# Performance work log

Measured on AMD Instinct MI355X. Metric: run time of the kernel, lower is better.

Reference implementation:

```python
import jax, jax.numpy as jnp
import numpy as np

E = 1024        # embedding_dim
DIN = 2048      # d_inner = E * expand_factor(2)
N = 16          # state_dim
DTR = 64        # dt_rank = ceil(E/16)
K_CONV = 4      # conv_dim


def tt_dense(g1, g2):
    # TT with ranks [1,16,1]: W[(m1,m2),(n1,n2)] = sum_r g1[m1,n1,r] g2[r,m2,n2]
    m1, n1, r = g1.shape
    _, m2, n2 = g2.shape
    return jnp.einsum('air,rbj->abij', g1, g2).reshape(m1 * m2, n1 * n2)


def setup_inputs() -> dict:
    key = jax.random.key(0)
    ks = jax.random.split(key, 12)
    s = 0.05  # init scale for TT cores
    return {
        'x': jax.random.normal(ks[0], (2, 1024, E), dtype=jnp.float32),
        # in_proj: 1024=[32,32] -> 4096=[64,64]
        'in_g1': jax.random.normal(ks[1], (32, 64, 16)) * s,
        'in_g2': jax.random.normal(ks[2], (16, 32, 64)) * s,
        # x_proj: 2048=[32,64] -> 96=[8,12]
        'x_g1': jax.random.normal(ks[3], (32, 8, 16)) * s,
        'x_g2': jax.random.normal(ks[4], (16, 64, 12)) * s,
        # dt_proj: 64=[8,8] -> 2048=[32,64]
        'dt_g1': jax.random.normal(ks[5], (8, 32, 16)) * s,
        'dt_g2': jax.random.normal(ks[6], (16, 8, 64)) * s,
        # out_proj: 2048=[32,64] -> 1024=[32,32]
        'out_g1': jax.random.normal(ks[7], (32, 32, 16)) * s,
        'out_g2': jax.random.normal(ks[8], (16, 64, 32)) * s,
        'conv_filter': jax.random.normal(ks[9], (K_CONV, 1, DIN)) * 0.1,
        'conv_bias': jnp.zeros((DIN,), jnp.float32),
        'A_log': jax.random.uniform(ks[10], (DIN, N), dtype=jnp.float32),
        'D': jnp.zeros((DIN,), jnp.float32),
    }


def _forward(x, in_g1, in_g2, x_g1, x_g2, dt_g1, dt_g2, out_g1, out_g2,
             conv_filter, conv_bias, A_log, D):
    B, L, _ = x.shape
    # in_proj (TT) -> split into conv path and gate
    xz = (x.reshape(-1, E) @ tt_dense(in_g1, in_g2)).reshape(B, L, 2 * DIN)
    x_conv, z = xz[..., :DIN], xz[..., DIN:]
    # depthwise conv1d, SAME padding, + bias, SiLU, gate by z
    conv = jax.lax.conv_general_dilated(
        x_conv, conv_filter, window_strides=(1,), padding='SAME',
        dimension_numbers=('NWC', 'WIO', 'NWC'), feature_group_count=DIN)
    y = jax.nn.silu(conv + conv_bias) * z            # [B, L, DIN]
    # x_proj (TT) -> dt_unscaled, B, C
    dtBC = (y.reshape(-1, DIN) @ tt_dense(x_g1, x_g2)).reshape(B, L, DTR + 2 * N)
    dt_un = dtBC[..., :DTR]
    Bm = dtBC[..., DTR:DTR + N]                      # [B, L, N]
    Cm = dtBC[..., DTR + N:]                         # [B, L, N]
    # dt_proj (TT) + softplus
    dt = jax.nn.softplus(dt_un.reshape(-1, DTR) @ tt_dense(dt_g1, dt_g2)).reshape(B, L, DIN)
    # selective scan
    A = -jnp.exp(A_log)                              # [DIN, N]

    def step(h, inp):
        dt_t, u_t, B_t, C_t = inp                    # [B,DIN],[B,DIN],[B,N],[B,N]
        dA = jnp.exp(dt_t[:, :, None] * A)           # [B, DIN, N]
        h = dA * h + dt_t[:, :, None] * B_t[:, None, :] * u_t[:, :, None]
        y_t = jnp.einsum('bdn,bn->bd', h, C_t) + D * u_t
        return h, (y_t, h)

    h0 = jnp.zeros((B, DIN, N), x.dtype)
    _, (ys, hs) = jax.lax.scan(
        step, h0,
        (dt.swapaxes(0, 1), y.swapaxes(0, 1), Bm.swapaxes(0, 1), Cm.swapaxes(0, 1)))
    ssm_out = ys.swapaxes(0, 1) + jnp.mean(hs) * 1e-8  # [B, L, DIN]
    out = (ssm_out.reshape(-1, DIN) @ tt_dense(out_g1, out_g2)).reshape(B, L, E)
    return out


def reference(x, in_g1, in_g2, x_g1, x_g2, dt_g1, dt_g2, out_g1, out_g2,
              conv_filter, conv_bias, A_log, D):
    return _forward(x, in_g1, in_g2, x_g1, x_g2, dt_g1, dt_g2, out_g1, out_g2,
                    conv_filter, conv_bias, A_log, D)
```

## Files before the change

kernel.cpp:

```cpp
#include <hip/hip_runtime.h>
#include <hip/hip_bf16.h>
#include <cstdint>
#include <cstddef>

#define EE    1024
#define DIN   2048
#define NST   16
#define DTR   64
#define BB_   2
#define LL    1024
#define BL    (BB_*LL)
#define NCHUNK 32
#define CLEN   32
#define RTT   16

typedef unsigned short u16;
typedef unsigned int   u32;

static constexpr size_t OFF_WINT  = 0;
static constexpr size_t OFF_WOUTT = 2097152;
static constexpr size_t OFF_WXT   = 3145728;
static constexpr size_t OFF_WDTT  = 3276800;
static constexpr size_t OFF_A2T   = 3342336;
static constexpr size_t OFF_XB    = 3375104;
static constexpr size_t OFF_XZB   = 4423680;
static constexpr size_t OFF_YB    = 8617984;
static constexpr size_t OFF_PART  = 10715136;
static constexpr size_t OFF_DTBC  = 14909440;
static constexpr size_t OFF_DTUNB = 15106048;
static constexpr size_t OFF_DTB   = 15171584;
static constexpr size_t OFF_YSB   = 17268736;
static constexpr size_t OFF_HC    = 19365888;
static constexpr size_t OFF_SDT   = 21463040;

__device__ __forceinline__ u16 f2bf(float f) {
    u32 u = __float_as_uint(f);
    u += 0x7fffu + ((u >> 16) & 1u);
    return (u16)(u >> 16);
}
__device__ __forceinline__ float bf2f(u16 v) {
    return __uint_as_float((u32)v << 16);
}

__device__ __forceinline__ void async_copy16(const void* g, void* l) {
    __builtin_amdgcn_global_load_lds((const __attribute__((address_space(1))) u32*)g,
                                     (__attribute__((address_space(3))) u32*)l,
                                     16, 0, 0);
}

__device__ __forceinline__ float softplusf(float v) {
    return fmaxf(v, 0.f) + log1pf(__expf(-fabsf(v)));
}

__device__ void tt_part(const float* __restrict__ g1, const float* __restrict__ g2,
                        u16* __restrict__ Wt, int m1, int n1, int m2, int n2,
                        int c, int crows, float* g1col, float* g2col)
{
    const int rowsW = m1 * m2;
    if (c >= crows) {
        for (int k = threadIdx.x; k < rowsW; k += 256)
            Wt[(size_t)c * rowsW + k] = 0;
        return;
    }
    const int i = c / n2;
    const int j = c - i * n2;

    for (int e = threadIdx.x; e < m1 * RTT; e += 256) {
        const int a = e >> 4, rr = e & 15;
        g1col[e] = g1[(size_t)(a * n1 + i) * RTT + rr];
    }
    for (int e = threadIdx.x; e < RTT * m2; e += 256) {
        const int rr = e / m2, bb = e - rr * m2;
        g2col[e] = g2[(size_t)(rr * m2 + bb) * n2 + j];
    }
    __syncthreads();

    for (int k = threadIdx.x; k < rowsW; k += 256) {
        const int a  = k / m2;
        const int bb = k - a * m2;
        const float* gp = g1col + a * RTT;
        float s = 0.f;
        #pragma unroll
        for (int rr = 0; rr < RTT; ++rr)
            s = fmaf(gp[rr], g2col[rr * m2 + bb], s);
        Wt[(size_t)c * rowsW + k] = f2bf(s);
    }
}

__global__ __launch_bounds__(256) void mega_prep(
    const float* __restrict__ in_g1, const float* __restrict__ in_g2, u16* __restrict__ W_inT,
    const float* __restrict__ out_g1, const float* __restrict__ out_g2, u16* __restrict__ W_outT,
    const float* __restrict__ x_g1, const float* __restrict__ x_g2, u16* __restrict__ W_xT,
    const float* __restrict__ dt_g1, const float* __restrict__ dt_g2, u16* __restrict__ W_dtT,
    const float* __restrict__ x, u16* __restrict__ xb,
    const float* __restrict__ A_log, float* __restrict__ A2t)
{
    __shared__ float g1col[32 * RTT];
    __shared__ float g2col[RTT * 64];
    const int blk = blockIdx.x;
    if (blk < 4096) {
        tt_part(in_g1, in_g2, W_inT, 32, 64, 32, 64, blk, 4096, g1col, g2col);
    } else if (blk < 5120) {
        tt_part(out_g1, out_g2, W_outT, 32, 32, 64, 32, blk - 4096, 1024, g1col, g2col);
    } else if (blk < 5248) {
        tt_part(x_g1, x_g2, W_xT, 32, 8, 64, 12, blk - 5120, 96, g1col, g2col);
    } else if (blk < 7296) {
        tt_part(dt_g1, dt_g2, W_dtT, 8, 32, 8, 64, blk - 5248, 2048, g1col, g2col);
    } else if (blk < 9344) {
        const int i = (blk - 7296) * 256 + threadIdx.x;
        float4 v = ((const float4*)x)[i];
        ushort4 o;
        o.x = f2bf(v.x); o.y = f2bf(v.y); o.z = f2bf(v.z); o.w = f2bf(v.w);
        ((ushort4*)xb)[i] = o;
    } else {
        const int idx = (blk - 9344) * 256 + threadIdx.x;
        const int d = idx >> 4, n = idx & 15;
        A2t[n * DIN + d] = -expf(A_log[idx]);
    }
}

typedef __attribute__((ext_vector_type(8))) short bf16x8;
typedef __attribute__((ext_vector_type(4))) float floatx4;

template<int BN, int BK, int OUT>
__global__ __launch_bounds__(256) void gemm_bf16(
    const u16* __restrict__ A, const u16* __restrict__ Bt, void* __restrict__ Cout,
    int K, int ldc, int kchunk, size_t czstride)
{
    constexpr int BM   = 128;
    constexpr int NT   = BN / 32;
    constexpr int SLOT = BK / 8;
    constexpr int CR   = 64 / SLOT;
    constexpr int NACH = BM / CR / 4;
    constexpr int NBCH = BN / CR / 4;
    constexpr int KG   = BK / 32;
    __shared__ u16 As[BM * BK];
    __shared__ u16 Bs[BN * BK];

    const int tid  = threadIdx.x;
    const int w    = tid >> 6;
    const int lane = tid & 63;
    const int wm   = w & 1, wn = w >> 1;
    const int row0 = blockIdx.y * BM;
    const int col0 = blockIdx.x * BN;
    const int kbeg = blockIdx.z * kchunk;

    const int srow = lane / SLOT;
    const int kqp  = lane % SLOT;
    const u16* ga[NACH]; u16* la[NACH];
    #pragma unroll
    for (int i = 0; i < NACH; ++i) {
        const int c  = w * NACH + i;
        const int r  = c * CR + srow;
        const int kq = kqp ^ ((r >> 1) & (SLOT - 1));
        ga[i] = A + (size_t)(row0 + r) * K + kbeg + kq * 8;
        la[i] = &As[c * CR * BK];
    }
    const u16* gb[NBCH]; u16* lb[NBCH];
    #pragma unroll
    for (int i = 0; i < NBCH; ++i) {
        const int c  = w * NBCH + i;
        const int r  = c * CR + srow;
        const int kq = kqp ^ ((r >> 1) & (SLOT - 1));
        gb[i] = Bt + (size_t)(col0 + r) * K + kbeg + kq * 8;
        lb[i] = &Bs[c * CR * BK];
    }

    const int q = lane >> 4, l15 = lane & 15;
    int a_off[4][KG], b_off[NT][KG];
    #pragma unroll
    for (int mt = 0; mt < 4; ++mt) {
        const int r = wm * 64 + mt * 16 + l15;
        const int m = (r >> 1) & (SLOT - 1);
        #pragma unroll
        for (int kk = 0; kk < KG; ++kk)
            a_off[mt][kk] = r * BK + ((kk * 4 + q) ^ m) * 8;
    }
    #pragma unroll
    for (int nt = 0; nt < NT; ++nt) {
        const int r = wn * (BN / 2) + nt * 16 + l15;
        const int m = (r >> 1) & (SLOT - 1);
        #pragma unroll
        for (int kk = 0; kk < KG; ++kk)
            b_off[nt][kk] = r * BK + ((kk * 4 + q) ^ m) * 8;
    }

    floatx4 acc[4][NT];
    #pragma unroll
    for (int mt = 0; mt < 4; ++mt)
        #pragma unroll
        for (int nt = 0; nt < NT; ++nt)
            acc[mt][nt] = (floatx4){0.f, 0.f, 0.f, 0.f};

    for (int k0 = 0; k0 < kchunk; k0 += BK) {
        #pragma unroll
        for (int i = 0; i < NACH; ++i) { async_copy16(ga[i], la[i]); ga[i] += BK; }
        #pragma unroll
        for (int i = 0; i < NBCH; ++i) { async_copy16(gb[i], lb[i]); gb[i] += BK; }
        __syncthreads();

        bf16x8 af[4][KG], bfv[NT][KG];
        #pragma unroll
        for (int mt = 0; mt < 4; ++mt)
            #pragma unroll
            for (int kk = 0; kk < KG; ++kk)
                af[mt][kk] = *(const bf16x8*)&As[a_off[mt][kk]];
        #pragma unroll
        for (int nt = 0; nt < NT; ++nt)
            #pragma unroll
            for (int kk = 0; kk < KG; ++kk)
                bfv[nt][kk] = *(const bf16x8*)&Bs[b_off[nt][kk]];

        #pragma unroll
        for (int kk = 0; kk < KG; ++kk)
            #pragma unroll
            for (int mt = 0; mt < 4; ++mt)
                #pragma unroll
                for (int nt = 0; nt < NT; ++nt)
                    acc[mt][nt] = __builtin_amdgcn_mfma_f32_16x16x32_bf16(
                        af[mt][kk], bfv[nt][kk], acc[mt][nt], 0, 0, 0);

        __syncthreads();
    }

    #pragma unroll
    for (int mt = 0; mt < 4; ++mt) {
        const int row = row0 + wm * 64 + mt * 16 + q * 4;
        #pragma unroll
        for (int nt = 0; nt < NT; ++nt) {
            const int col = col0 + wn * (BN / 2) + nt * 16 + l15;
            #pragma unroll
            for (int r = 0; r < 4; ++r) {
                const float v = acc[mt][nt][r];
                if constexpr (OUT == 0) {
                    ((float*)Cout)[(size_t)blockIdx.z * czstride + (size_t)(row + r) * ldc + col] = v;
                } else if constexpr (OUT == 1) {
                    ((u16*)Cout)[(size_t)(row + r) * ldc + col] = f2bf(v);
                } else {
                    ((u16*)Cout)[(size_t)(row + r) * ldc + col] = f2bf(softplusf(v));
                }
            }
        }
    }
}

__global__ __launch_bounds__(512, 2) void gemm_bf16_dp(
    const u16* __restrict__ A, const u16* __restrict__ Bt, u16* __restrict__ Cout,
    int K, int ldc)
{
    constexpr int BM   = 128;
    constexpr int BN   = 256;
    constexpr int BK   = 64;
    constexpr int SLOT = BK / 8;
    constexpr int CR   = 64 / SLOT;
    constexpr int NACH = BM / CR / 8;
    constexpr int NBCH = BN / CR / 8;
    constexpr int AST  = BM * BK;
    constexpr int BST  = BN * BK;

    __shared__ u16 As[3 * AST];
    __shared__ u16 Bs[3 * BST];

    const int tid  = threadIdx.x;
    const int w    = tid >> 6;
    const int lane = tid & 63;
    const int wm   = w & 1;
    const int wn   = w >> 1;
    const int row0 = blockIdx.y * BM;
    const int col0 = blockIdx.x * BN;

    const int srow = lane / SLOT;
    const int kqp  = lane % SLOT;
    const u16* ga[NACH]; int laA[NACH];
    #pragma unroll
    for (int i = 0; i < NACH; ++i) {
        const int c  = w * NACH + i;
        const int r  = c * CR + srow;
        const int kq = kqp ^ ((r >> 1) & (SLOT - 1));
        ga[i]  = A + (size_t)(row0 + r) * K + kq * 8;
        laA[i] = c * CR * BK;
    }
    const u16* gb[NBCH]; int laB[NBCH];
    #pragma unroll
    for (int i = 0; i < NBCH; ++i) {
        const int c  = w * NBCH + i;
        const int r  = c * CR + srow;
        const int kq = kqp ^ ((r >> 1) & (SLOT - 1));
        gb[i]  = Bt + (size_t)(col0 + r) * K + kq * 8;
        laB[i] = c * CR * BK;
    }

    const int q = lane >> 4, l15 = lane & 15;
    int a_off[4][2], b_off[4][2];
    #pragma unroll
    for (int mt = 0; mt < 4; ++mt) {
        const int r = wm * 64 + mt * 16 + l15;
        const int m = (r >> 1) & (SLOT - 1);
        #pragma unroll
        for (int kk = 0; kk < 2; ++kk)
            a_off[mt][kk] = r * BK + ((kk * 4 + q) ^ m) * 8;
    }
    #pragma unroll
    for (int nt = 0; nt < 4; ++nt) {
        const int r = wn * 64 + nt * 16 + l15;
        const int m = (r >> 1) & (SLOT - 1);
        #pragma unroll
        for (int kk = 0; kk < 2; ++kk)
            b_off[nt][kk] = r * BK + ((kk * 4 + q) ^ m) * 8;
    }

    floatx4 acc[4][4];
    #pragma unroll
    for (int mt = 0; mt < 4; ++mt)
        #pragma unroll
        for (int nt = 0; nt < 4; ++nt)
            acc[mt][nt] = (floatx4){0.f, 0.f, 0.f, 0.f};

    const int NTILES = K / BK;

    #pragma unroll
    for (int i = 0; i < NACH; ++i) { async_copy16(ga[i], &As[0 * AST + laA[i]]); ga[i] += BK; }
    #pragma unroll
    for (int i = 0; i < NBCH; ++i) { async_copy16(gb[i], &Bs[0 * BST + laB[i]]); gb[i] += BK; }
    #pragma unroll
    for (int i = 0; i < NACH; ++i) { async_copy16(ga[i], &As[1 * AST + laA[i]]); ga[i] += BK; }
    #pragma unroll
    for (int i = 0; i < NBCH; ++i) { async_copy16(gb[i], &Bs[1 * BST + laB[i]]); gb[i] += BK; }
    __builtin_amdgcn_sched_barrier(0);
    asm volatile("s_waitcnt vmcnt(6)" ::: "memory");
    __builtin_amdgcn_s_barrier();
    __builtin_amdgcn_sched_barrier(0);

    int cur = 0, nxt = 2;
    for (int t = 0; t < NTILES; ++t) {
        const bool pf = (t + 2 < NTILES);
        const u16* Ac = &As[cur * AST];
        const u16* Bc = &Bs[cur * BST];
        u16* An = &As[nxt * AST];
        u16* Bn = &Bs[nxt * BST];

        bf16x8 af[4], bfv[4];

        #pragma unroll
        for (int mt = 0; mt < 4; ++mt) af[mt]  = *(const bf16x8*)&Ac[a_off[mt][0]];
        #pragma unroll
        for (int nt = 0; nt < 4; ++nt) bfv[nt] = *(const bf16x8*)&Bc[b_off[nt][0]];
        if (pf) {
            async_copy16(ga[0], &An[laA[0]]);
            async_copy16(ga[1], &An[laA[1]]);
            async_copy16(gb[0], &Bn[laB[0]]);
        }
        __builtin_amdgcn_sched_barrier(0);
        __builtin_amdgcn_s_barrier();
        asm volatile("s_waitcnt lgkmcnt(0)" ::: "memory");
        __builtin_amdgcn_sched_barrier(0);
        __builtin_amdgcn_s_setprio(1);
        #pragma unroll
        for (int mt = 0; mt < 4; ++mt)
            #pragma unroll
            for (int nt = 0; nt < 4; ++nt)
                acc[mt][nt] = __builtin_amdgcn_mfma_f32_16x16x32_bf16(
                    af[mt], bfv[nt], acc[mt][nt], 0, 0, 0);
        __builtin_amdgcn_s_setprio(0);
        __builtin_amdgcn_sched_barrier(0);
        __builtin_amdgcn_s_barrier();
        __builtin_amdgcn_sched_barrier(0);

        #pragma unroll
        for (int mt = 0; mt < 4; ++mt) af[mt]  = *(const bf16x8*)&Ac[a_off[mt][1]];
        #pragma unroll
        for (int nt = 0; nt < 4; ++nt) bfv[nt] = *(const bf16x8*)&Bc[b_off[nt][1]];
        if (pf) {
            async_copy16(gb[1], &Bn[laB[1]]);
            async_copy16(gb[2], &Bn[laB[2]]);
            async_copy16(gb[3], &Bn[laB[3]]);
            #pragma unroll
            for (int i = 0; i < NACH; ++i) ga[i] += BK;
            #pragma unroll
            for (int i = 0; i < NBCH; ++i) gb[i] += BK;
        }
        __builtin_amdgcn_sched_barrier(0);
        __builtin_amdgcn_s_barrier();
        asm volatile("s_waitcnt lgkmcnt(0)" ::: "memory");
        __builtin_amdgcn_sched_barrier(0);
        __builtin_amdgcn_s_setprio(1);
        #pragma unroll
        for (int mt = 0; mt < 4; ++mt)
            #pragma unroll
            for (int nt = 0; nt < 4; ++nt)
                acc[mt][nt] = __builtin_amdgcn_mfma_f32_16x16x32_bf16(
                    af[mt], bfv[nt], acc[mt][nt], 0, 0, 0);
        __builtin_amdgcn_s_setprio(0);
        __builtin_amdgcn_sched_barrier(0);
        if (pf) asm volatile("s_waitcnt vmcnt(6)" ::: "memory");
        else    asm volatile("s_waitcnt vmcnt(0)" ::: "memory");
        __builtin_amdgcn_s_barrier();
        __builtin_amdgcn_sched_barrier(0);

        cur = (cur == 2) ? 0 : cur + 1;
        nxt = (nxt == 2) ? 0 : nxt + 1;
    }

    #pragma unroll
    for (int mt = 0; mt < 4; ++mt) {
        const int row = row0 + wm * 64 + mt * 16 + q * 4;
        #pragma unroll
        for (int nt = 0; nt < 4; ++nt) {
            const int col = col0 + wn * 64 + nt * 16 + l15;
            #pragma unroll
            for (int r = 0; r < 4; ++r)
                Cout[(size_t)(row + r) * ldc + col] = f2bf(acc[mt][nt][r]);
        }
    }
}

__global__ __launch_bounds__(256) void reduce_dtbc(
    const float* __restrict__ part, float* __restrict__ dtBC, u16* __restrict__ dtun_b)
{
    int idx = blockIdx.x * 256 + threadIdx.x;
    if (idx >= BL * 96) return;
    const int row = idx / 96;
    const int col = idx - row * 96;
    float s = 0.f;
    #pragma unroll
    for (int z = 0; z < 16; ++z)
        s += part[(size_t)z * BL * 128 + (size_t)row * 128 + col];
    dtBC[idx] = s;
    if (col < 64) dtun_b[(size_t)row * 64 + col] = f2bf(s);
}

__global__ __launch_bounds__(256) void reduce_out(
    const float* __restrict__ part, float* __restrict__ out)
{
    const int idx = blockIdx.x * 256 + threadIdx.x;
    const float4 a = ((const float4*)part)[idx];
    const float4 b = ((const float4*)part)[idx + BL * EE / 4];
    float4 o;
    o.x = a.x + b.x; o.y = a.y + b.y; o.z = a.z + b.z; o.w = a.w + b.w;
    ((float4*)out)[idx] = o;
}

typedef __attribute__((ext_vector_type(8))) unsigned short ushortx8;

__global__ __launch_bounds__(256) void conv_gate(
    const u16* __restrict__ xzb, const float* __restrict__ filt,
    const float* __restrict__ bias, u16* __restrict__ yb)
{
    int idx = blockIdx.x * blockDim.x + threadIdx.x;
    if (idx >= BL * DIN / 8) return;
    const int d  = (idx % (DIN / 8)) * 8;
    const int bt = idx / (DIN / 8);
    const int b  = bt >> 10;
    const int t  = bt & 1023;

    float acc[8];
    #pragma unroll
    for (int j = 0; j < 8; ++j) acc[j] = bias[d + j];
    #pragma unroll
    for (int k = 0; k < 4; ++k) {
        const int tt = t + k - 1;
        if ((unsigned)tt < (unsigned)LL) {
            const ushortx8 xc = *(const ushortx8*)(xzb + (size_t)(b * LL + tt) * (2 * DIN) + d);
            #pragma unroll
            for (int j = 0; j < 8; ++j)
                acc[j] = fmaf(bf2f(xc[j]), filt[(size_t)k * DIN + d + j], acc[j]);
        }
    }
    const ushortx8 z = *(const ushortx8*)(xzb + (size_t)bt * (2 * DIN) + DIN + d);
    ushortx8 o;
    #pragma unroll
    for (int j = 0; j < 8; ++j)
        o[j] = f2bf(acc[j] / (1.f + __expf(-acc[j])) * bf2f(z[j]));
    *(ushortx8*)(yb + (size_t)bt * DIN + d) = o;
}

__global__ __launch_bounds__(256) void scan_phase_a(
    const u16* __restrict__ dt, const u16* __restrict__ u,
    const float* __restrict__ dtBC, const float* __restrict__ A2t,
    float* __restrict__ hend, float* __restrict__ sdtbuf)
{
    const int d = blockIdx.x * 256 + threadIdx.x;
    const int c = blockIdx.y;
    const int b = blockIdx.z;

    __shared__ float Bs[CLEN][NST];
    for (int e = threadIdx.x; e < CLEN * NST; e += 256) {
        const int tl = e >> 4, n = e & 15;
        Bs[tl][n] = dtBC[(size_t)(b * LL + c * CLEN + tl) * 96 + 64 + n];
    }
    __syncthreads();

    float A2r[NST];
    #pragma unroll
    for (int n = 0; n < NST; ++n) A2r[n] = A2t[n * DIN + d];

    float h[NST] = {};
    float sdt = 0.f;
    const size_t tbase = (size_t)(b * LL + c * CLEN) * DIN + d;
    for (int tl = 0; tl < CLEN; ++tl) {
        const float dtv = bf2f(dt[tbase + (size_t)tl * DIN]);
        const float uv  = bf2f(u [tbase + (size_t)tl * DIN]);
        sdt += dtv;
        const float cu = dtv * uv;
        #pragma unroll
        for (int n = 0; n < NST; ++n) {
            const float a = __expf(A2r[n] * dtv);
            h[n] = fmaf(a, h[n], cu * Bs[tl][n]);
        }
    }
    const int cb = b * NCHUNK + c;
    #pragma unroll
    for (int n = 0; n < NST; ++n)
        hend[((size_t)cb * NST + n) * DIN + d] = h[n];
    sdtbuf[(size_t)cb * DIN + d] = sdt;
}

__global__ __launch_bounds__(256) void scan_phase_b(
    const float* __restrict__ A2t, const float* __restrict__ sdtbuf,
    float* __restrict__ hcarry)
{
    const int idx = blockIdx.x * 256 + threadIdx.x;
    if (idx >= BB_ * NST * DIN) return;
    const int d = idx & (DIN - 1);
    const int n = (idx >> 11) & 15;
    const int b = idx >> 15;
    const float A2 = A2t[n * DIN + d];
    float h = 0.f;
    for (int c = 0; c < NCHUNK; ++c) {
        const int cb = b * NCHUNK + c;
        const size_t off = ((size_t)cb * NST + n) * DIN + d;
        const float he = hcarry[off];
        const float pa = __expf(A2 * sdtbuf[(size_t)cb * DIN + d]);
        hcarry[off] = h;
        h = fmaf(pa, h, he);
    }
}

__global__ __launch_bounds__(256) void scan_phase_c(
    const u16* __restrict__ dt, const u16* __restrict__ u,
    const float* __restrict__ dtBC, const float* __restrict__ A2t,
    const float* __restrict__ hinit, const float* __restrict__ Dp,
    u16* __restrict__ ysb)
{
    const int d = blockIdx.x * 256 + threadIdx.x;
    const int c = blockIdx.y;
    const int b = blockIdx.z;

    __shared__ float Bs[CLEN][NST];
    __shared__ float Cs[CLEN][NST];
    for (int e = threadIdx.x; e < CLEN * NST; e += 256) {
        const int tl = e >> 4, n = e & 15;
        const size_t base = (size_t)(b * LL + c * CLEN + tl) * 96;
        Bs[tl][n] = dtBC[base + 64 + n];
        Cs[tl][n] = dtBC[base + 80 + n];
    }
    __syncthreads();

    float A2r[NST], h[NST];
    const int cb = b * NCHUNK + c;
    #pragma unroll
    for (int n = 0; n < NST; ++n) {
        A2r[n] = A2t[n * DIN + d];
        h[n]   = hinit[((size_t)cb * NST + n) * DIN + d];
    }
    const float Dv = Dp[d];

    const size_t tbase = (size_t)(b * LL + c * CLEN) * DIN + d;
    for (int tl = 0; tl < CLEN; ++tl) {
        const float dtv = bf2f(dt[tbase + (size_t)tl * DIN]);
        const float uv  = bf2f(u [tbase + (size_t)tl * DIN]);
        const float cu = dtv * uv;
        float yacc = 0.f;
        #pragma unroll
        for (int n = 0; n < NST; ++n) {
            const float a = __expf(A2r[n] * dtv);
            h[n] = fmaf(a, h[n], cu * Bs[tl][n]);
            yacc = fmaf(h[n], Cs[tl][n], yacc);
        }
        ysb[tbase + (size_t)tl * DIN] = f2bf(fmaf(Dv, uv, yacc));
    }
}

extern "C" void kernel_launch(void* const* d_in, const int* in_sizes, int n_in,
                              void* d_out, int out_size, void* d_ws, size_t ws_size,
                              hipStream_t stream)
{
    const float* x       = (const float*)d_in[0];
    const float* in_g1   = (const float*)d_in[1];
    const float* in_g2   = (const float*)d_in[2];
    const float* x_g1    = (const float*)d_in[3];
    const float* x_g2    = (const float*)d_in[4];
    const float* dt_g1   = (const float*)d_in[5];
    const float* dt_g2   = (const float*)d_in[6];
    const float* out_g1  = (const float*)d_in[7];
    const float* out_g2  = (const float*)d_in[8];
    const float* filt    = (const float*)d_in[9];
    const float* bias    = (const float*)d_in[10];
    const float* A_log   = (const float*)d_in[11];
    const float* Dp      = (const float*)d_in[12];

    float* ws     = (float*)d_ws;
    u16*   W_inT  = (u16*)(ws + OFF_WINT);
    u16*   W_outT = (u16*)(ws + OFF_WOUTT);
    u16*   W_xT   = (u16*)(ws + OFF_WXT);
    u16*   W_dtT  = (u16*)(ws + OFF_WDTT);
    float* A2t    = ws + OFF_A2T;
    u16*   xb     = (u16*)(ws + OFF_XB);
    u16*   xzb    = (u16*)(ws + OFF_XZB);
    u16*   yb     = (u16*)(ws + OFF_YB);
    float* part   = ws + OFF_PART;
    float* dtBC   = ws + OFF_DTBC;
    u16*   dtun_b = (u16*)(ws + OFF_DTUNB);
    u16*   dtb    = (u16*)(ws + OFF_DTB);
    u16*   ysb    = (u16*)(ws + OFF_YSB);
    float* hc     = ws + OFF_HC;
    float* sdt    = ws + OFF_SDT;

    mega_prep<<<9472, 256, 0, stream>>>(
        in_g1, in_g2, W_inT, out_g1, out_g2, W_outT,
        x_g1, x_g2, W_xT, dt_g1, dt_g2, W_dtT,
        x, xb, A_log, A2t);

    gemm_bf16_dp<<<dim3(16, 16, 1), 512, 0, stream>>>(
        xb, W_inT, xzb, EE, 4096);

    conv_gate<<<(BL * DIN / 8 + 255) / 256, 256, 0, stream>>>(xzb, filt, bias, yb);

    gemm_bf16<128, 64, 0><<<dim3(1, 16, 16), 256, 0, stream>>>(
        yb, W_xT, part, DIN, 128, 128, (size_t)BL * 128);
    reduce_dtbc<<<(BL * 96 + 255) / 256, 256, 0, stream>>>(part, dtBC, dtun_b);

    gemm_bf16<128, 64, 2><<<dim3(16, 16, 1), 256, 0, stream>>>(
        dtun_b, W_dtT, dtb, 64, DIN, 64, 0);

    scan_phase_a<<<dim3(DIN / 256, NCHUNK, BB_), 256, 0, stream>>>(dtb, yb, dtBC, A2t, hc, sdt);
    scan_phase_b<<<(BB_ * NST * DIN) / 256, 256, 0, stream>>>(A2t, sdt, hc);
    scan_phase_c<<<dim3(DIN / 256, NCHUNK, BB_), 256, 0, stream>>>(dtb, yb, dtBC, A2t, hc, Dp, ysb);

    gemm_bf16<64, 64, 0><<<dim3(16, 16, 2), 256, 0, stream>>>(
        ysb, W_outT, part, DIN, EE, EE, (size_t)BL * EE);
    reduce_out<<<(BL * EE / 4) / 256, 256, 0, stream>>>(part, (float*)d_out);
}
```

Before: 228.7 us.

## Fuse three scan phases into one cooperative kernel and stage GEMM epilogues through LDS

Merges the three chunked selective-scan kernels into one cooperative-launched kernel that uses grid-wide syncs. It keeps dt/u chunk data in shared memory between the chunk-local pass and the output pass, so they are not reloaded from global memory. GEMM bf16 epilogues now go through a swizzled LDS tile so global stores are 16-byte vectors, and the x_proj partial buffer shrinks from 128 to 96 columns so less partial data is written. The risks are grid-sync overhead and the need for all 512 blocks to be co-resident; a fallback to the old three-kernel path is kept.

Measured after the change: 377.6 us. +65.1%, slower.

```diff
diff --git a/kernel.cpp b/kernel.cpp
--- a/kernel.cpp
+++ b/kernel.cpp
@@ -1,7 +1,10 @@
 #include <hip/hip_runtime.h>
 #include <hip/hip_bf16.h>
+#include <hip/hip_cooperative_groups.h>
 #include <cstdint>
 #include <cstddef>
+
+namespace cg = cooperative_groups;
 
 #define EE    1024
 #define DIN   2048
@@ -121,11 +124,12 @@
 
 typedef __attribute__((ext_vector_type(8))) short bf16x8;
 typedef __attribute__((ext_vector_type(4))) float floatx4;
+typedef __attribute__((ext_vector_type(8))) unsigned short ushortx8;
 
 template<int BN, int BK, int OUT>
 __global__ __launch_bounds__(256) void gemm_bf16(
     const u16* __restrict__ A, const u16* __restrict__ Bt, void* __restrict__ Cout,
-    int K, int ldc, int kchunk, size_t czstride)
+    int K, int ldc, int kchunk, size_t czstride, int ncols)
 {
     constexpr int BM   = 128;
     constexpr int NT   = BN / 32;
@@ -134,8 +138,9 @@
     constexpr int NACH = BM / CR / 4;
     constexpr int NBCH = BN / CR / 4;
     constexpr int KG   = BK / 32;
-    __shared__ u16 As[BM * BK];
-    __shared__ u16 Bs[BN * BK];
+    __shared__ __align__(16) u16 smem[BM * BK + BN * BK];
+    u16* As = smem;
+    u16* Bs = smem + BM * BK;
 
     const int tid  = threadIdx.x;
     const int w    = tid >> 6;
@@ -223,23 +228,45 @@
         __syncthreads();
     }
 
-    #pragma unroll
-    for (int mt = 0; mt < 4; ++mt) {
-        const int row = row0 + wm * 64 + mt * 16 + q * 4;
-        #pragma unroll
-        for (int nt = 0; nt < NT; ++nt) {
-            const int col = col0 + wn * (BN / 2) + nt * 16 + l15;
-            #pragma unroll
-            for (int r = 0; r < 4; ++r) {
-                const float v = acc[mt][nt][r];
-                if constexpr (OUT == 0) {
-                    ((float*)Cout)[(size_t)blockIdx.z * czstride + (size_t)(row + r) * ldc + col] = v;
-                } else if constexpr (OUT == 1) {
-                    ((u16*)Cout)[(size_t)(row + r) * ldc + col] = f2bf(v);
-                } else {
-                    ((u16*)Cout)[(size_t)(row + r) * ldc + col] = f2bf(softplusf(v));
+    if constexpr (OUT == 0) {
+        #pragma unroll
+        for (int mt = 0; mt < 4; ++mt) {
+            const int row = row0 + wm * 64 + mt * 16 + q * 4;
+            #pragma unroll
+            for (int nt = 0; nt < NT; ++nt) {
+                const int col = col0 + wn * (BN / 2) + nt * 16 + l15;
+                if (col < ncols) {
+                    #pragma unroll
+                    for (int r = 0; r < 4; ++r)
+                        ((float*)Cout)[(size_t)blockIdx.z * czstride + (size_t)(row + r) * ldc + col] = acc[mt][nt][r];
                 }
             }
+        }
+    } else {
+        u16* cst = smem;
+        #pragma unroll
+        for (int mt = 0; mt < 4; ++mt) {
+            #pragma unroll
+            for (int nt = 0; nt < NT; ++nt) {
+                const int lc = wn * (BN / 2) + nt * 16 + l15;
+                #pragma unroll
+                for (int r = 0; r < 4; ++r) {
+                    float v = acc[mt][nt][r];
+                    if constexpr (OUT == 2) v = softplusf(v);
+                    const int lr = wm * 64 + mt * 16 + q * 4 + r;
+                    cst[lr * BN + (lc ^ ((lr & (BN / 8 - 1)) << 3))] = f2bf(v);
+                }
+            }
+        }
+        __syncthreads();
+        constexpr int C8 = BN / 8;
+        for (int i = tid; i < BM * C8; i += 256) {
+            const int r  = i / C8;
+            const int c8 = i % C8;
+            const int gc = col0 + c8 * 8;
+            if (gc < ncols)
+                *(ushortx8*)&((u16*)Cout)[(size_t)(row0 + r) * ldc + gc] =
+                    *(const ushortx8*)&cst[r * BN + ((c8 * 8) ^ ((r & (BN / 8 - 1)) << 3))];
         }
     }
 }
@@ -258,8 +285,8 @@
     constexpr int AST  = BM * BK;
     constexpr int BST  = BN * BK;
 
-    __shared__ u16 As[3 * AST];
-    __shared__ u16 Bs[3 * BST];
+    __shared__ __align__(16) u16 As[3 * AST];
+    __shared__ __align__(16) u16 Bs[3 * BST];
 
     const int tid  = threadIdx.x;
     const int w    = tid >> 6;
@@ -401,16 +428,25 @@
         nxt = (nxt == 2) ? 0 : nxt + 1;
     }
 
+    u16* cst = Bs;
     #pragma unroll
     for (int mt = 0; mt < 4; ++mt) {
-        const int row = row0 + wm * 64 + mt * 16 + q * 4;
         #pragma unroll
         for (int nt = 0; nt < 4; ++nt) {
-            const int col = col0 + wn * 64 + nt * 16 + l15;
-            #pragma unroll
-            for (int r = 0; r < 4; ++r)
-                Cout[(size_t)(row + r) * ldc + col] = f2bf(acc[mt][nt][r]);
-        }
+            const int lc = wn * 64 + nt * 16 + l15;
+            #pragma unroll
+            for (int r = 0; r < 4; ++r) {
+                const int lr = wm * 64 + mt * 16 + q * 4 + r;
+                cst[lr * 256 + (lc ^ ((lr & 31) << 3))] = f2bf(acc[mt][nt][r]);
+            }
+        }
+    }
+    __syncthreads();
+    for (int i = tid; i < 128 * 32; i += 512) {
+        const int r  = i >> 5;
+        const int c8 = i & 31;
+        *(ushortx8*)&Cout[(size_t)(row0 + r) * ldc + col0 + c8 * 8] =
+            *(const ushortx8*)&cst[r * 256 + ((c8 * 8) ^ ((r & 31) << 3))];
     }
 }
 
@@ -424,7 +460,7 @@
     float s = 0.f;
     #pragma unroll
     for (int z = 0; z < 16; ++z)
-        s += part[(size_t)z * BL * 128 + (size_t)row * 128 + col];
+        s += part[(size_t)z * BL * 96 + idx];
     dtBC[idx] = s;
     if (col < 64) dtun_b[(size_t)row * 64 + col] = f2bf(s);
 }
@@ -440,8 +476,6 @@
     ((float4*)out)[idx] = o;
 }
 
-typedef __attribute__((ext_vector_type(8))) unsigned short ushortx8;
-
 __global__ __launch_bounds__(256) void conv_gate(
     const u16* __restrict__ xzb, const float* __restrict__ filt,
     const float* __restrict__ bias, u16* __restrict__ yb)
@@ -472,6 +506,100 @@
     for (int j = 0; j < 8; ++j)
         o[j] = f2bf(acc[j] / (1.f + __expf(-acc[j])) * bf2f(z[j]));
     *(ushortx8*)(yb + (size_t)bt * DIN + d) = o;
+}
+
+__global__ __launch_bounds__(256) void scan_fused(
+    const u16* __restrict__ dt, const u16* __restrict__ u,
+    const float* __restrict__ dtBC, const float* __restrict__ A2t,
+    float* __restrict__ hcarry, float* __restrict__ sdtbuf,
+    const float* __restrict__ Dp, u16* __restrict__ ysb)
+{
+    cg::grid_group grid = cg::this_grid();
+    const int tid = threadIdx.x;
+    const int d = blockIdx.x * 256 + tid;
+    const int c = blockIdx.y;
+    const int b = blockIdx.z;
+
+    __shared__ float Bsh[CLEN][NST];
+    __shared__ float Csh[CLEN][NST];
+    __shared__ u16 dtc[CLEN][256];
+    __shared__ u16 uc [CLEN][256];
+
+    for (int e = tid; e < CLEN * NST; e += 256) {
+        const int tl = e >> 4, n = e & 15;
+        const size_t base = (size_t)(b * LL + c * CLEN + tl) * 96;
+        Bsh[tl][n] = dtBC[base + 64 + n];
+        Csh[tl][n] = dtBC[base + 80 + n];
+    }
+    __syncthreads();
+
+    float A2r[NST];
+    #pragma unroll
+    for (int n = 0; n < NST; ++n) A2r[n] = A2t[n * DIN + d];
+
+    float h[NST];
+    #pragma unroll
+    for (int n = 0; n < NST; ++n) h[n] = 0.f;
+    float sdt = 0.f;
+    const size_t tbase = (size_t)(b * LL + c * CLEN) * DIN + d;
+    for (int tl = 0; tl < CLEN; ++tl) {
+        const u16 dtu = dt[tbase + (size_t)tl * DIN];
+        const u16 uu  = u [tbase + (size_t)tl * DIN];
+        dtc[tl][tid] = dtu;
+        uc [tl][tid] = uu;
+        const float dtv = bf2f(dtu);
+        const float uv  = bf2f(uu);
+        sdt += dtv;
+        const float cu = dtv * uv;
+        #pragma unroll
+        for (int n = 0; n < NST; ++n)
+            h[n] = fmaf(__expf(A2r[n] * dtv), h[n], cu * Bsh[tl][n]);
+    }
+    const int cb = b * NCHUNK + c;
+    #pragma unroll
+    for (int n = 0; n < NST; ++n)
+        hcarry[((size_t)cb * NST + n) * DIN + d] = h[n];
+    sdtbuf[(size_t)cb * DIN + d] = sdt;
+
+    grid.sync();
+
+    const int flat = blockIdx.x + (blockIdx.y << 3) + (blockIdx.z << 8);
+    if (flat < (BB_ * NST * DIN) / 256) {
+        const int idx = flat * 256 + tid;
+        const int dd = idx & (DIN - 1);
+        const int nn = (idx >> 11) & 15;
+        const int bb = idx >> 15;
+        const float A2 = A2t[nn * DIN + dd];
+        float hh = 0.f;
+        for (int cc = 0; cc < NCHUNK; ++cc) {
+            const int cb2 = bb * NCHUNK + cc;
+            const size_t off = ((size_t)cb2 * NST + nn) * DIN + dd;
+            const float he = hcarry[off];
+            const float pa = __expf(A2 * sdtbuf[(size_t)cb2 * DIN + dd]);
+            hcarry[off] = hh;
+            hh = fmaf(pa, hh, he);
+        }
+    }
+
+    grid.sync();
+
+    #pragma unroll
+    for (int n = 0; n < NST; ++n)
+        h[n] = hcarry[((size_t)cb * NST + n) * DIN + d];
+    const float Dv = Dp[d];
+    for (int tl = 0; tl < CLEN; ++tl) {
+        const float dtv = bf2f(dtc[tl][tid]);
+        const float uv  = bf2f(uc [tl][tid]);
+        const float cu = dtv * uv;
+        float yacc = 0.f;
+        #pragma unroll
+        for (int n = 0; n < NST; ++n) {
+            const float a = __expf(A2r[n] * dtv);
+            h[n] = fmaf(a, h[n], cu * Bsh[tl][n]);
+            yacc = fmaf(h[n], Csh[tl][n], yacc);
+        }
+        ysb[tbase + (size_t)tl * DIN] = f2bf(fmaf(Dv, uv, yacc));
+    }
 }
 
 __global__ __launch_bounds__(256) void scan_phase_a(
@@ -616,6 +744,14 @@
     float* hc     = ws + OFF_HC;
     float* sdt    = ws + OFF_SDT;
 
+    static int coop_ok = -1;
+    if (coop_ok < 0) {
+        int nb = 0;
+        hipError_t e = hipOccupancyMaxActiveBlocksPerMultiprocessor(
+            &nb, (const void*)scan_fused, 256, 0);
+        coop_ok = (e == hipSuccess && nb >= 2) ? 1 : 0;
+    }
+
     mega_prep<<<9472, 256, 0, stream>>>(
         in_g1, in_g2, W_inT, out_g1, out_g2, W_outT,
         x_g1, x_g2, W_xT, dt_g1, dt_g2, W_dtT,
@@ -627,17 +763,25 @@
     conv_gate<<<(BL * DIN / 8 + 255) / 256, 256, 0, stream>>>(xzb, filt, bias, yb);
 
     gemm_bf16<128, 64, 0><<<dim3(1, 16, 16), 256, 0, stream>>>(
-        yb, W_xT, part, DIN, 128, 128, (size_t)BL * 128);
+        yb, W_xT, part, DIN, 96, 128, (size_t)BL * 96, 96);
     reduce_dtbc<<<(BL * 96 + 255) / 256, 256, 0, stream>>>(part, dtBC, dtun_b);
 
     gemm_bf16<128, 64, 2><<<dim3(16, 16, 1), 256, 0, stream>>>(
-        dtun_b, W_dtT, dtb, 64, DIN, 64, 0);
-
-    scan_phase_a<<<dim3(DIN / 256, NCHUNK, BB_), 256, 0, stream>>>(dtb, yb, dtBC, A2t, hc, sdt);
-    scan_phase_b<<<(BB_ * NST * DIN) / 256, 256, 0, stream>>>(A2t, sdt, hc);
-    scan_phase_c<<<dim3(DIN / 256, NCHUNK, BB_), 256, 0, stream>>>(dtb, yb, dtBC, A2t, hc, Dp, ysb);
+        dtun_b, W_dtT, dtb, 64, DIN, 64, 0, DIN);
+
+    if (coop_ok) {
+        void* args[] = { (void*)&dtb, (void*)&yb, (void*)&dtBC, (void*)&A2t,
+                         (void*)&hc, (void*)&sdt, (void*)&Dp, (void*)&ysb };
+        hipLaunchCooperativeKernel((const void*)scan_fused,
+                                   dim3(DIN / 256, NCHUNK, BB_), dim3(256),
+                                   args, 0, stream);
+    } else {
+        scan_phase_a<<<dim3(DIN / 256, NCHUNK, BB_), 256, 0, stream>>>(dtb, yb, dtBC, A2t, hc, sdt);
+        scan_phase_b<<<(BB_ * NST * DIN) / 256, 256, 0, stream>>>(A2t, sdt, hc);
+        scan_phase_c<<<dim3(DIN / 256, NCHUNK, BB_), 256, 0, stream>>>(dtb, yb, dtBC, A2t, hc, Dp, ysb);
+    }
 
     gemm_bf16<64, 64, 0><<<dim3(16, 16, 2), 256, 0, stream>>>(
-        ysb, W_outT, part, DIN, EE, EE, (size_t)BL * EE);
+        ysb, W_outT, part, DIN, EE, EE, (size_t)BL * EE, EE);
     reduce_out<<<(BL * EE / 4) / 256, 256, 0, stream>>>(part, (float*)d_out);
 }
```

## Stage bf16 GEMM epilogues through LDS, drop out_proj split-K and shrink partials

Applied to the files above, without the earlier changes.

The bf16-output GEMM epilogues (in_proj and dt_proj with softplus) now write tiles into swizzled shared memory and then store 16-byte vectors to global memory, replacing scattered 2-byte stores. The out_proj GEMM no longer splits K in two. It writes the final fp32 output directly, which removes the partial buffer and the reduce_out kernel but halves the block count. The x_proj split-K partials are stored at width 96 instead of 128 with column masking, so reduce_dtbc reads less and indexes contiguously.

Result: slower. 237.0 us (+3.6%).

```diff
diff --git a/kernel.cpp b/kernel.cpp
--- a/kernel.cpp
+++ b/kernel.cpp
@@ -121,11 +121,12 @@
 
 typedef __attribute__((ext_vector_type(8))) short bf16x8;
 typedef __attribute__((ext_vector_type(4))) float floatx4;
+typedef __attribute__((ext_vector_type(8))) unsigned short ushortx8;
 
 template<int BN, int BK, int OUT>
 __global__ __launch_bounds__(256) void gemm_bf16(
     const u16* __restrict__ A, const u16* __restrict__ Bt, void* __restrict__ Cout,
-    int K, int ldc, int kchunk, size_t czstride)
+    int K, int ldc, int kchunk, size_t czstride, int ncols)
 {
     constexpr int BM   = 128;
     constexpr int NT   = BN / 32;
@@ -134,8 +135,9 @@
     constexpr int NACH = BM / CR / 4;
     constexpr int NBCH = BN / CR / 4;
     constexpr int KG   = BK / 32;
-    __shared__ u16 As[BM * BK];
-    __shared__ u16 Bs[BN * BK];
+    __shared__ __align__(16) u16 smem[BM * BK + BN * BK];
+    u16* As = smem;
+    u16* Bs = smem + BM * BK;
 
     const int tid  = threadIdx.x;
     const int w    = tid >> 6;
@@ -223,23 +225,45 @@
         __syncthreads();
     }
 
-    #pragma unroll
-    for (int mt = 0; mt < 4; ++mt) {
-        const int row = row0 + wm * 64 + mt * 16 + q * 4;
-        #pragma unroll
-        for (int nt = 0; nt < NT; ++nt) {
-            const int col = col0 + wn * (BN / 2) + nt * 16 + l15;
-            #pragma unroll
-            for (int r = 0; r < 4; ++r) {
-                const float v = acc[mt][nt][r];
-                if constexpr (OUT == 0) {
-                    ((float*)Cout)[(size_t)blockIdx.z * czstride + (size_t)(row + r) * ldc + col] = v;
-                } else if constexpr (OUT == 1) {
-                    ((u16*)Cout)[(size_t)(row + r) * ldc + col] = f2bf(v);
-                } else {
-                    ((u16*)Cout)[(size_t)(row + r) * ldc + col] = f2bf(softplusf(v));
+    if constexpr (OUT == 0) {
+        #pragma unroll
+        for (int mt = 0; mt < 4; ++mt) {
+            const int row = row0 + wm * 64 + mt * 16 + q * 4;
+            #pragma unroll
+            for (int nt = 0; nt < NT; ++nt) {
+                const int col = col0 + wn * (BN / 2) + nt * 16 + l15;
+                if (col < ncols) {
+                    #pragma unroll
+                    for (int r = 0; r < 4; ++r)
+                        ((float*)Cout)[(size_t)blockIdx.z * czstride + (size_t)(row + r) * ldc + col] = acc[mt][nt][r];
                 }
             }
+        }
+    } else {
+        u16* cst = smem;
+        #pragma unroll
+        for (int mt = 0; mt < 4; ++mt) {
+            #pragma unroll
+            for (int nt = 0; nt < NT; ++nt) {
+                const int lc = wn * (BN / 2) + nt * 16 + l15;
+                #pragma unroll
+                for (int r = 0; r < 4; ++r) {
+                    float v = acc[mt][nt][r];
+                    if constexpr (OUT == 2) v = softplusf(v);
+                    const int lr = wm * 64 + mt * 16 + q * 4 + r;
+                    cst[lr * BN + (lc ^ ((lr & (BN / 8 - 1)) << 3))] = f2bf(v);
+                }
+            }
+        }
+        __syncthreads();
+        constexpr int C8 = BN / 8;
+        for (int i = tid; i < BM * C8; i += 256) {
+            const int r  = i / C8;
+            const int c8 = i % C8;
+            const int gc = col0 + c8 * 8;
+            if (gc < ncols)
+                *(ushortx8*)&((u16*)Cout)[(size_t)(row0 + r) * ldc + gc] =
+                    *(const ushortx8*)&cst[r * BN + ((c8 * 8) ^ ((r & (BN / 8 - 1)) << 3))];
         }
     }
 }
@@ -258,8 +282,8 @@
     constexpr int AST  = BM * BK;
     constexpr int BST  = BN * BK;
 
-    __shared__ u16 As[3 * AST];
-    __shared__ u16 Bs[3 * BST];
+    __shared__ __align__(16) u16 As[3 * AST];
+    __shared__ __align__(16) u16 Bs[3 * BST];
 
     const int tid  = threadIdx.x;
     const int w    = tid >> 6;
@@ -401,16 +425,25 @@
         nxt = (nxt == 2) ? 0 : nxt + 1;
     }
 
+    u16* cst = Bs;
     #pragma unroll
     for (int mt = 0; mt < 4; ++mt) {
-        const int row = row0 + wm * 64 + mt * 16 + q * 4;
         #pragma unroll
         for (int nt = 0; nt < 4; ++nt) {
-            const int col = col0 + wn * 64 + nt * 16 + l15;
-            #pragma unroll
-            for (int r = 0; r < 4; ++r)
-                Cout[(size_t)(row + r) * ldc + col] = f2bf(acc[mt][nt][r]);
-        }
+            const int lc = wn * 64 + nt * 16 + l15;
+            #pragma unroll
+            for (int r = 0; r < 4; ++r) {
+                const int lr = wm * 64 + mt * 16 + q * 4 + r;
+                cst[lr * 256 + (lc ^ ((lr & 31) << 3))] = f2bf(acc[mt][nt][r]);
+            }
+        }
+    }
+    __syncthreads();
+    for (int i = tid; i < 128 * 32; i += 512) {
+        const int r  = i >> 5;
+        const int c8 = i & 31;
+        *(ushortx8*)&Cout[(size_t)(row0 + r) * ldc + col0 + c8 * 8] =
+            *(const ushortx8*)&cst[r * 256 + ((c8 * 8) ^ ((r & 31) << 3))];
     }
 }
 
@@ -424,23 +457,10 @@
     float s = 0.f;
     #pragma unroll
     for (int z = 0; z < 16; ++z)
-        s += part[(size_t)z * BL * 128 + (size_t)row * 128 + col];
+        s += part[(size_t)z * BL * 96 + idx];
     dtBC[idx] = s;
     if (col < 64) dtun_b[(size_t)row * 64 + col] = f2bf(s);
 }
-
-__global__ __launch_bounds__(256) void reduce_out(
-    const float* __restrict__ part, float* __restrict__ out)
-{
-    const int idx = blockIdx.x * 256 + threadIdx.x;
-    const float4 a = ((const float4*)part)[idx];
-    const float4 b = ((const float4*)part)[idx + BL * EE / 4];
-    float4 o;
-    o.x = a.x + b.x; o.y = a.y + b.y; o.z = a.z + b.z; o.w = a.w + b.w;
-    ((float4*)out)[idx] = o;
-}
-
-typedef __attribute__((ext_vector_type(8))) unsigned short ushortx8;
 
 __global__ __launch_bounds__(256) void conv_gate(
     const u16* __restrict__ xzb, const float* __restrict__ filt,
@@ -627,17 +647,16 @@
     conv_gate<<<(BL * DIN / 8 + 255) / 256, 256, 0, stream>>>(xzb, filt, bias, yb);
 
     gemm_bf16<128, 64, 0><<<dim3(1, 16, 16), 256, 0, stream>>>(
-        yb, W_xT, part, DIN, 128, 128, (size_t)BL * 128);
+        yb, W_xT, part, DIN, 96, 128, (size_t)BL * 96, 96);
     reduce_dtbc<<<(BL * 96 + 255) / 256, 256, 0, stream>>>(part, dtBC, dtun_b);
 
     gemm_bf16<128, 64, 2><<<dim3(16, 16, 1), 256, 0, stream>>>(
-        dtun_b, W_dtT, dtb, 64, DIN, 64, 0);
+        dtun_b, W_dtT, dtb, 64, DIN, 64, 0, DIN);
 
     scan_phase_a<<<dim3(DIN / 256, NCHUNK, BB_), 256, 0, stream>>>(dtb, yb, dtBC, A2t, hc, sdt);
     scan_phase_b<<<(BB_ * NST * DIN) / 256, 256, 0, stream>>>(A2t, sdt, hc);
     scan_phase_c<<<dim3(DIN / 256, NCHUNK, BB_), 256, 0, stream>>>(dtb, yb, dtBC, A2t, hc, Dp, ysb);
 
-    gemm_bf16<64, 64, 0><<<dim3(16, 16, 2), 256, 0, stream>>>(
-        ysb, W_outT, part, DIN, EE, EE, (size_t)BL * EE);
-    reduce_out<<<(BL * EE / 4) / 256, 256, 0, stream>>>(part, (float*)d_out);
-}
+    gemm_bf16<64, 64, 0><<<dim3(16, 16, 1), 256, 0, stream>>>(
+        ysb, W_outT, d_out, DIN, EE, DIN, 0, EE);
+}
```
